# Kernel optimization log

Hardware: AMD Instinct MI355X
Metric: run time of the kernel (lower is better)

The kernel has to match this reference:

```python
import jax, jax.numpy as jnp
import numpy as np

# dims from init_kwargs
B, T = 64, 128
CB, DB = 8, 256
IN_DIM = CB + DB            # 264
H_STATE = 512
NUM_HEADS = 4
NUM_SHIFT = 3
M = 128                     # memory content size (slot width)
A = 2048                    # number of memory addresses
READ_SIZE = NUM_HEADS * M   # 512
PARAMS_PER_HEAD = M + 1 + 1 + NUM_SHIFT + 1 + 2 * M  # key,beta,g,shift,gamma,erase,add = 390
UPDATE_SIZE = NUM_HEADS * PARAMS_PER_HEAD             # 1560
EPS = 1e-8


def setup_inputs() -> dict:
    key = jax.random.key(0)
    ks = jax.random.split(key, 4)
    w = lambda k, sh: jax.random.normal(k, sh, jnp.float32) * 0.02
    return {
        "x": jax.random.normal(ks[0], (B, T, IN_DIM), jnp.float32),
        "W_state": w(ks[1], (IN_DIM + H_STATE + READ_SIZE, H_STATE)),
        "b_state": jnp.zeros((H_STATE,), jnp.float32),
        "W_out": w(ks[2], (H_STATE, DB)),
        "b_out": jnp.zeros((DB,), jnp.float32),
        "W_upd": w(ks[3], (H_STATE, UPDATE_SIZE)),
        "b_upd": jnp.zeros((UPDATE_SIZE,), jnp.float32),
    }


def _ntm_step(params, carry, x_t):
    W_state, b_state, W_out, b_out, W_upd, b_upd = params
    h, wt, mem = carry  # h [B,S], wt [B,H,A], mem [B,M,A]

    # --- read from memory with previous attention ---
    read = jnp.einsum('bma,bha->bhm', mem, wt).reshape(B, READ_SIZE)

    # --- controller ---
    ctrl_in = jnp.concatenate([x_t, h, read], axis=-1)
    h_new = jax.nn.sigmoid(ctrl_in @ W_state + b_state)
    out = jax.nn.sigmoid(h_new @ W_out + b_out)
    upd = (h_new @ W_upd + b_upd).reshape(B, NUM_HEADS, PARAMS_PER_HEAD)

    # --- split interface parameters per head ---
    k_vec = upd[..., :M]                                              # key [B,H,M]
    beta = jax.nn.softplus(upd[..., M:M + 1])                         # key strength
    g = jax.nn.sigmoid(upd[..., M + 1:M + 2])                         # interpolation gate
    shift = jax.nn.softmax(upd[..., M + 2:M + 2 + NUM_SHIFT], axis=-1)
    gamma = 1.0 + jax.nn.softplus(upd[..., M + 2 + NUM_SHIFT:M + 3 + NUM_SHIFT])
    erase = jax.nn.sigmoid(upd[..., M + 3 + NUM_SHIFT:2 * M + 3 + NUM_SHIFT])
    add = jnp.tanh(upd[..., 2 * M + 3 + NUM_SHIFT:])

    # --- content addressing: cosine similarity + sharpened softmax ---
    dots = jnp.einsum('bhm,bma->bha', k_vec, mem)
    k_norm = jnp.linalg.norm(k_vec, axis=-1, keepdims=True)           # [B,H,1]
    m_norm = jnp.linalg.norm(mem, axis=1)[:, None, :]                 # [B,1,A]
    sim = dots / (k_norm * m_norm + EPS)
    wc = jax.nn.softmax(beta * sim, axis=-1)

    # --- gate with previous attention ---
    wg = g * wc + (1.0 - g) * wt

    # --- circular convolutional shift (small fixed loop over NUM_SHIFT) ---
    center = NUM_SHIFT // 2
    shifted = jnp.stack([jnp.roll(wg, s - center, axis=-1) for s in range(NUM_SHIFT)], axis=2)  # [B,H,S,A]
    ws = jnp.einsum('bhs,bhsa->bha', shift, shifted)

    # --- sharpening ---
    wp = jnp.power(ws + EPS, gamma)
    wt_new = wp / jnp.sum(wp, axis=-1, keepdims=True)

    # --- memory erase / add ---
    erase_term = jnp.prod(1.0 - jnp.einsum('bhm,bha->bhma', erase, wt_new), axis=1)  # [B,M,A]
    add_term = jnp.einsum('bhm,bha->bma', add, wt_new)
    mem_new = mem * erase_term + add_term

    return (h_new, wt_new, mem_new), out


def reference(x, W_state, b_state, W_out, b_out, W_upd, b_upd):
    # init_state (matches torch module): h=ones, wt one-hot at address 0, mem=0.01
    h0 = jnp.ones((B, H_STATE), jnp.float32)
    wt0 = jnp.zeros((B, NUM_HEADS, A), jnp.float32).at[:, :, 0].set(1.0)
    mem0 = jnp.full((B, M, A), 0.01, jnp.float32)
    params = (W_state, b_state, W_out, b_out, W_upd, b_upd)

    def step(carry, x_t):
        return _ntm_step(params, carry, x_t)

    _, outs = jax.lax.scan(step, (h0, wt0, mem0), jnp.swapaxes(x, 0, 1))
    return jnp.swapaxes(outs, 0, 1)  # [B, T, DB]
```

## Files before the change

### kernel.cpp

```cpp
#include <hip/hip_runtime.h>
#include <math.h>

#define BB 64
#define TT 128
#define DBX 256
#define IND 264
#define HS 512
#define NH 4
#define MMM 128
#define AAA 2048
#define PPH 390
#define NCOLS (DBX + NH*PPH)
#define KTOT (IND + HS + HS)
#define KSPL 8
#define KCH  161
#define EPSF 1e-8f

__device__ __forceinline__ float sigmf(float x){ return 1.0f/(1.0f+expf(-x)); }
__device__ __forceinline__ float softplusf(float x){ return (x > 20.0f) ? x : log1pf(expf(x)); }

__global__ void k_init(float* __restrict__ hT, float* __restrict__ readT,
                       float* __restrict__ wt, float* __restrict__ mem){
  int i = blockIdx.x*blockDim.x + threadIdx.x;
  int stride = gridDim.x*blockDim.x;
  for (int idx=i; idx<BB*MMM*AAA; idx+=stride) mem[idx]=0.01f;
  for (int idx=i; idx<HS*BB; idx+=stride){ hT[idx]=1.0f; readT[idx]=0.01f; }
  for (int idx=i; idx<BB*NH*AAA; idx+=stride) wt[idx] = ((idx & (AAA-1))==0)?1.0f:0.0f;
}

__global__ __launch_bounds__(256) void k_tx(const float* __restrict__ x, float* __restrict__ xT){
  int b = blockIdx.x;
  for (int f = threadIdx.x; f < TT*IND; f += 256)
    xT[(size_t)f*BB + b] = x[(size_t)b*TT*IND + f];
}

__global__ __launch_bounds__(256) void k1_state(
    const float* __restrict__ xT, const float* __restrict__ Wst,
    const float* __restrict__ hTp, const float* __restrict__ readTp,
    float* __restrict__ hpart, float* __restrict__ wcsum, float* __restrict__ wpsum, int t)
{
  int tid = threadIdx.x, wave = tid>>6, lane = tid&63;
  int ks = blockIdx.y;
  int j0 = blockIdx.x*16 + wave*4;
  if (blockIdx.x==0 && ks==0){
    wcsum[tid] = 0.0f;
    wpsum[tid] = 0.0f;
  }
  float a0=0,a1=0,a2=0,a3=0;
  int k0 = ks*KCH, kend = k0+KCH;

  #define K1STEP(AEXPR) { float aV=(AEXPR); \
      float4 wv = *(const float4*)(Wst + (size_t)k*HS + j0); \
      a0 += aV*wv.x; a1 += aV*wv.y; a2 += aV*wv.z; a3 += aV*wv.w; }

  {int s = k0, e = kend<IND?kend:IND;
   #pragma unroll 4
   for (int k=s;k<e;++k) K1STEP(xT[((size_t)t*IND + k)*BB + lane]); }
  {int s = k0>IND?k0:IND, e = kend<(IND+HS)?kend:(IND+HS);
   #pragma unroll 4
   for (int k=s;k<e;++k) K1STEP(hTp[(k-IND)*BB + lane]); }
  {int s = k0>(IND+HS)?k0:(IND+HS), e = kend;
   #pragma unroll 4
   for (int k=s;k<e;++k) K1STEP(readTp[(k-IND-HS)*BB + lane]); }
  #undef K1STEP

  float* hp = hpart + (size_t)ks*HS*BB + (size_t)j0*BB + lane;
  hp[0]    = a0;
  hp[BB]   = a1;
  hp[2*BB] = a2;
  hp[3*BB] = a3;
}

__global__ __launch_bounds__(512) void k2h(
    const float* __restrict__ hpart, const float* __restrict__ bst, float* __restrict__ hTn)
{
  int idx = blockIdx.x*512 + threadIdx.x;
  float v = 0.0f;
  #pragma unroll
  for (int ks=0; ks<KSPL; ++ks) v += hpart[(size_t)ks*HS*BB + idx];
  hTn[idx] = sigmf(v + bst[idx>>6]);
}

__global__ __launch_bounds__(256) void k2_outupd(
    const float* __restrict__ hTn,
    const float* __restrict__ Wout, const float* __restrict__ bout,
    const float* __restrict__ Wupd, const float* __restrict__ bupd,
    float* __restrict__ out,
    float* __restrict__ kvec_t, float* __restrict__ beta, float* __restrict__ gbuf,
    float* __restrict__ gam, float* __restrict__ shraw,
    float* __restrict__ erase, float* __restrict__ addb, int t)
{
  __shared__ float part[4][8][BB];
  int tid = threadIdx.x, ks = tid>>6, lane = tid&63;
  int c0 = blockIdx.x*8;
  bool isout = (c0 < DBX);
  size_t strd = isout ? (size_t)DBX : (size_t)(NH*PPH);
  const float* wbase = isout ? (Wout + c0) : (Wupd + (c0 - DBX));
  bool valid = (c0 < NCOLS);

  float acc[8] = {0,0,0,0,0,0,0,0};
  if (valid){
    int k0 = ks*128;
    #pragma unroll 4
    for (int k=k0; k<k0+128; ++k){
      float a = hTn[k*BB + lane];
      const float4* w4 = (const float4*)(wbase + (size_t)k*strd);
      float4 wa = w4[0], wb = w4[1];
      acc[0]+=a*wa.x; acc[1]+=a*wa.y; acc[2]+=a*wa.z; acc[3]+=a*wa.w;
      acc[4]+=a*wb.x; acc[5]+=a*wb.y; acc[6]+=a*wb.z; acc[7]+=a*wb.w;
    }
  }
  #pragma unroll
  for (int u=0; u<8; ++u) part[ks][u][lane] = acc[u];
  __syncthreads();
  if (!valid) return;

  for (int idx=tid; idx<8*BB; idx+=256){
    int u = idx>>6, b = idx&63;
    int c = c0+u;
    float v = part[0][u][b] + part[1][u][b] + part[2][u][b] + part[3][u][b];
    if (isout){
      out[((size_t)b*TT + t)*DBX + c] = sigmf(v + bout[c]);
    } else {
      int u2 = c - DBX;
      int hh = u2 / PPH;
      int p  = u2 - hh*PPH;
      v += bupd[u2];
      if (p < MMM)            kvec_t[b*HS + p*NH + hh] = v;
      else if (p == MMM)      beta[b*NH+hh] = softplusf(v);
      else if (p == MMM+1)    gbuf[b*NH+hh] = sigmf(v);
      else if (p <  MMM+5)    shraw[(b*NH+hh)*3 + (p-(MMM+2))] = v;
      else if (p == MMM+5)    gam[b*NH+hh] = 1.0f + softplusf(v);
      else if (p <  2*MMM+6)  erase[b*HS + hh*MMM + (p-(MMM+6))] = sigmf(v);
      else                    addb[b*HS + hh*MMM + (p-(2*MMM+6))] = tanhf(v);
    }
  }
}

__global__ __launch_bounds__(512) void k_dotsP(
    const float* __restrict__ mem, const float* __restrict__ kvec_t,
    float* __restrict__ dpart, float* __restrict__ n2part)
{
  int b = blockIdx.x, s = blockIdx.y, z = blockIdx.z, tid = threadIdx.x;
  __shared__ __align__(16) float klt[128];
  if (tid < 128) klt[tid] = kvec_t[b*HS + z*128 + tid];
  __syncthreads();
  int a = s*512 + tid;
  const float* mp = mem + (size_t)b*MMM*AAA + (size_t)(z*32)*AAA + a;
  const float4* k4 = (const float4*)klt;
  float a0=0,a1=0,a2=0,a3=0,n2=0;
  #pragma unroll 8
  for (int m=0; m<32; ++m){
    float mv = mp[(size_t)m*AAA];
    float4 kv = k4[m];
    a0 += kv.x*mv; a1 += kv.y*mv; a2 += kv.z*mv; a3 += kv.w*mv;
    n2 += mv*mv;
  }
  size_t base = ((size_t)(z*BB+b)*NH)*AAA + a;
  dpart[base]        = a0;
  dpart[base+AAA]    = a1;
  dpart[base+2*AAA]  = a2;
  dpart[base+3*AAA]  = a3;
  n2part[(size_t)(z*BB+b)*AAA + a] = n2;
}

__global__ __launch_bounds__(512) void k_dotsF(
    const float* __restrict__ dpart, const float* __restrict__ n2part,
    const float* __restrict__ kvec_t, const float* __restrict__ beta,
    float* __restrict__ ebuf, float* __restrict__ wcsum)
{
  int b = blockIdx.x, s = blockIdx.y, tid = threadIdx.x;
  __shared__ float red[HS];
  __shared__ float kn[NH];
  __shared__ float rsum[8*NH];
  float kv = kvec_t[b*HS + tid];
  red[tid] = kv*kv;
  __syncthreads();
  #pragma unroll
  for (int off=256; off>=4; off>>=1){
    if (tid < off) red[tid] += red[tid+off];
    __syncthreads();
  }
  if (tid < NH) kn[tid] = sqrtf(red[tid]);
  __syncthreads();

  int a = s*512 + tid;
  float d[NH] = {0,0,0,0};
  float n2 = 0.0f;
  #pragma unroll
  for (int z=0; z<4; ++z){
    size_t base = ((size_t)(z*BB+b)*NH)*AAA + a;
    d[0] += dpart[base];
    d[1] += dpart[base+AAA];
    d[2] += dpart[base+2*AAA];
    d[3] += dpart[base+3*AAA];
    n2   += n2part[(size_t)(z*BB+b)*AAA + a];
  }
  float mn = sqrtf(n2);
  int wid = tid >> 6, lane = tid & 63;
  #pragma unroll
  for (int hh=0; hh<NH; ++hh){
    float sim = d[hh]/(kn[hh]*mn + EPSF);
    float e = expf(beta[b*NH+hh]*sim);
    ebuf[((size_t)(b*NH+hh))*AAA + a] = e;
    float v = e;
    #pragma unroll
    for (int off=32; off>0; off>>=1) v += __shfl_xor(v, off);
    if (lane==0) rsum[wid*NH+hh] = v;
  }
  __syncthreads();
  if (tid < NH){
    float s2 = 0.0f;
    #pragma unroll
    for (int w=0; w<8; ++w) s2 += rsum[w*NH+tid];
    atomicAdd(&wcsum[b*NH+tid], s2);
  }
}

__global__ __launch_bounds__(512) void k_shift(
    const float* __restrict__ ebuf, const float* __restrict__ wcsum,
    const float* __restrict__ gbuf, const float* __restrict__ shraw,
    const float* __restrict__ gam, const float* __restrict__ wt,
    float* __restrict__ wpb, float* __restrict__ wpsum)
{
  int b = blockIdx.x, s = blockIdx.y, tid = threadIdx.x;
  int a = s*512 + tid;
  int am1 = (a + AAA - 1) & (AAA-1);
  int ap1 = (a + 1) & (AAA-1);
  __shared__ float sh[NH*3], gl[NH], gml[NH], winv[NH];
  __shared__ float rsum[8*NH];
  if (tid < NH){
    int hh = tid;
    float s0=shraw[(b*NH+hh)*3], s1=shraw[(b*NH+hh)*3+1], s2=shraw[(b*NH+hh)*3+2];
    float mx = fmaxf(s0, fmaxf(s1, s2));
    float e0=expf(s0-mx), e1=expf(s1-mx), e2=expf(s2-mx);
    float inv = 1.0f/(e0+e1+e2);
    sh[hh*3+0]=e0*inv; sh[hh*3+1]=e1*inv; sh[hh*3+2]=e2*inv;
    gl[hh]  = gbuf[b*NH+hh];
    gml[hh] = gam[b*NH+hh];
    winv[hh]= 1.0f/wcsum[b*NH+hh];
  }
  __syncthreads();
  int wid = tid >> 6, lane = tid & 63;
  #pragma unroll
  for (int hh=0; hh<NH; ++hh){
    const float* eb = ebuf + ((size_t)(b*NH+hh))*AAA;
    const float* wb = wt   + ((size_t)(b*NH+hh))*AAA;
    float inv = winv[hh], g = gl[hh];
    float s0 = sh[hh*3+0], s1 = sh[hh*3+1], s2 = sh[hh*3+2];
    float wgm1 = g*eb[am1]*inv + (1.0f-g)*wb[am1];
    float wg0  = g*eb[a]  *inv + (1.0f-g)*wb[a];
    float wgp1 = g*eb[ap1]*inv + (1.0f-g)*wb[ap1];
    float ws = s0*wgp1 + s1*wg0 + s2*wgm1;
    float wp = powf(ws + EPSF, gml[hh]);
    wpb[((size_t)(b*NH+hh))*AAA + a] = wp;
    float v = wp;
    #pragma unroll
    for (int off=32; off>0; off>>=1) v += __shfl_xor(v, off);
    if (lane==0) rsum[wid*NH+hh] = v;
  }
  __syncthreads();
  if (tid < NH){
    float s3 = 0.0f;
    #pragma unroll
    for (int w=0; w<8; ++w) s3 += rsum[w*NH+tid];
    atomicAdd(&wpsum[b*NH+tid], s3);
  }
}

__global__ __launch_bounds__(512) void k_updAB(
    float* __restrict__ mem, const float* __restrict__ wpb, const float* __restrict__ wpsum,
    const float* __restrict__ erase, const float* __restrict__ addb,
    float* __restrict__ wt, float* __restrict__ readTn)
{
  __shared__ __align__(16) float wl[AAA*4];
  int b = blockIdx.x, my = blockIdx.y, tid = threadIdx.x;
  int wave = tid >> 6, lane = tid & 63;
  float winv[4];
  #pragma unroll
  for (int h=0;h<4;++h) winv[h] = 1.0f/wpsum[b*NH+h];
  #pragma unroll
  for (int c4=0;c4<4;++c4){
    int a = c4*512 + tid;
    float w0 = wpb[((size_t)(b*NH+0))*AAA + a]*winv[0];
    float w1 = wpb[((size_t)(b*NH+1))*AAA + a]*winv[1];
    float w2 = wpb[((size_t)(b*NH+2))*AAA + a]*winv[2];
    float w3 = wpb[((size_t)(b*NH+3))*AAA + a]*winv[3];
    wl[a*4+0]=w0; wl[a*4+1]=w1; wl[a*4+2]=w2; wl[a*4+3]=w3;
    if (my == 0){
      wt[((size_t)(b*NH+0))*AAA + a] = w0;
      wt[((size_t)(b*NH+1))*AAA + a] = w1;
      wt[((size_t)(b*NH+2))*AAA + a] = w2;
      wt[((size_t)(b*NH+3))*AAA + a] = w3;
    }
  }
  __syncthreads();

  int m0 = my*8 + wave, m1 = m0 + 64;
  float er0[4], ad0[4], er1[4], ad1[4];
  #pragma unroll
  for (int h=0;h<4;++h){
    er0[h] = erase[b*HS + h*MMM + m0];
    ad0[h] = addb [b*HS + h*MMM + m0];
    er1[h] = erase[b*HS + h*MMM + m1];
    ad1[h] = addb [b*HS + h*MMM + m1];
  }
  float* row0 = mem + (size_t)b*MMM*AAA + (size_t)m0*AAA;
  float* row1 = mem + (size_t)b*MMM*AAA + (size_t)m1*AAA;
  const float4* wl4 = (const float4*)wl;
  float r00=0,r01=0,r02=0,r03=0, r10=0,r11=0,r12=0,r13=0;
  #pragma unroll 4
  for (int it=0; it<32; ++it){
    int a = it*64 + lane;
    float mv0 = row0[a], mv1 = row1[a];
    float4 w4 = wl4[a];
    float et0 = (1.0f - er0[0]*w4.x)*(1.0f - er0[1]*w4.y)
              * (1.0f - er0[2]*w4.z)*(1.0f - er0[3]*w4.w);
    float at0 = ad0[0]*w4.x + ad0[1]*w4.y + ad0[2]*w4.z + ad0[3]*w4.w;
    float n0 = mv0*et0 + at0;
    row0[a] = n0;
    r00 += n0*w4.x; r01 += n0*w4.y; r02 += n0*w4.z; r03 += n0*w4.w;
    float et1 = (1.0f - er1[0]*w4.x)*(1.0f - er1[1]*w4.y)
              * (1.0f - er1[2]*w4.z)*(1.0f - er1[3]*w4.w);
    float at1 = ad1[0]*w4.x + ad1[1]*w4.y + ad1[2]*w4.z + ad1[3]*w4.w;
    float n1 = mv1*et1 + at1;
    row1[a] = n1;
    r10 += n1*w4.x; r11 += n1*w4.y; r12 += n1*w4.z; r13 += n1*w4.w;
  }
  float rr[2][NH] = {{r00,r01,r02,r03},{r10,r11,r12,r13}};
  #pragma unroll
  for (int q=0; q<2; ++q){
    #pragma unroll
    for (int hh=0; hh<NH; ++hh){
      float v = rr[q][hh];
      #pragma unroll
      for (int off=32; off>0; off>>=1) v += __shfl_xor(v, off);
      rr[q][hh] = v;
    }
  }
  if (lane == 0){
    #pragma unroll
    for (int hh=0; hh<NH; ++hh){
      readTn[(size_t)(hh*MMM+m0)*BB + b] = rr[0][hh];
      readTn[(size_t)(hh*MMM+m1)*BB + b] = rr[1][hh];
    }
  }
}

extern "C" void kernel_launch(void* const* d_in, const int* in_sizes, int n_in,
                              void* d_out, int out_size, void* d_ws, size_t ws_size,
                              hipStream_t stream){
  const float* x    = (const float*)d_in[0];
  const float* Wst  = (const float*)d_in[1];
  const float* bst  = (const float*)d_in[2];
  const float* Wout = (const float*)d_in[3];
  const float* bout = (const float*)d_in[4];
  const float* Wupd = (const float*)d_in[5];
  const float* bupd = (const float*)d_in[6];
  float* out = (float*)d_out;

  float* p = (float*)d_ws;
  float* hT     = p; p += 2*HS*BB;
  float* readT  = p; p += 2*HS*BB;
  float* hpart  = p; p += KSPL*HS*BB;
  float* xT     = p; p += (size_t)TT*IND*BB;
  float* wt     = p; p += BB*NH*AAA;
  float* mem    = p; p += (size_t)BB*MMM*AAA;
  float* kvec_t = p; p += BB*HS;
  float* beta   = p; p += BB*NH;
  float* gbuf   = p; p += BB*NH;
  float* gam    = p; p += BB*NH;
  float* shraw  = p; p += BB*NH*3;
  float* erase  = p; p += BB*HS;
  float* addb   = p; p += BB*HS;
  float* ebuf   = p; p += BB*NH*AAA;
  float* wpb    = p; p += 4*(size_t)BB*NH*AAA;
  float* n2part = p; p += 4*BB*AAA;
  float* wcsum  = p; p += BB*NH;
  float* wpsum  = p; p += BB*NH;
  float* dpart  = wpb;

  k_init<<<2048, 256, 0, stream>>>(hT, readT, wt, mem);
  k_tx<<<BB, 256, 0, stream>>>(x, xT);
  for (int t=0; t<TT; ++t){
    const float* hTp = hT    + (t&1)*HS*BB;
    float* hTn       = hT    + ((t+1)&1)*HS*BB;
    const float* rTp = readT + (t&1)*HS*BB;
    float* rTn       = readT + ((t+1)&1)*HS*BB;
    k1_state<<<dim3(32,KSPL), 256, 0, stream>>>(xT, Wst, hTp, rTp, hpart, wcsum, wpsum, t);
    k2h<<<64, 512, 0, stream>>>(hpart, bst, hTn);
    k2_outupd<<<dim3(259), 256, 0, stream>>>(hTn, Wout, bout, Wupd, bupd, out,
        kvec_t, beta, gbuf, gam, shraw, erase, addb, t);
    k_dotsP<<<dim3(BB,4,4), 512, 0, stream>>>(mem, kvec_t, dpart, n2part);
    k_dotsF<<<dim3(BB,4), 512, 0, stream>>>(dpart, n2part, kvec_t, beta, ebuf, wcsum);
    k_shift<<<dim3(BB,4), 512, 0, stream>>>(ebuf, wcsum, gbuf, shraw, gam, wt, wpb, wpsum);
    k_updAB<<<dim3(BB,8), 512, 0, stream>>>(mem, wpb, wpsum, erase, addb, wt, rTn);
  }
}
```

Baseline: 10.36 ms.

## Fuse dot split-K kernels and move shift/sharpen into memory update kernel

The two-stage content-addressing dots (partial over M chunks, then finalize) become a single kernel that streams all 128 memory rows per address, which removes the dpart/n2part round trip through global memory. The shift, sharpen and normalization steps are folded into the erase/add update kernel, so each of the 8 blocks per batch redundantly recomputes the full attention in shared memory and no longer needs a global wpsum atomic. The wt buffer is double-buffered so the previous attention can be read while the new one is written. This trades two launches and extra global traffic per step for redundant per-block compute and a larger shared-memory footprint (64KB).

```diff
diff --git a/kernel.cpp b/kernel.cpp
--- a/kernel.cpp
+++ b/kernel.cpp
@@ -11,7 +11,6 @@
 #define AAA 2048
 #define PPH 390
 #define NCOLS (DBX + NH*PPH)
-#define KTOT (IND + HS + HS)
 #define KSPL 8
 #define KCH  161
 #define EPSF 1e-8f
@@ -20,12 +19,12 @@
 __device__ __forceinline__ float softplusf(float x){ return (x > 20.0f) ? x : log1pf(expf(x)); }
 
 __global__ void k_init(float* __restrict__ hT, float* __restrict__ readT,
-                       float* __restrict__ wt, float* __restrict__ mem){
+                       float* __restrict__ wt0, float* __restrict__ mem){
   int i = blockIdx.x*blockDim.x + threadIdx.x;
   int stride = gridDim.x*blockDim.x;
   for (int idx=i; idx<BB*MMM*AAA; idx+=stride) mem[idx]=0.01f;
   for (int idx=i; idx<HS*BB; idx+=stride){ hT[idx]=1.0f; readT[idx]=0.01f; }
-  for (int idx=i; idx<BB*NH*AAA; idx+=stride) wt[idx] = ((idx & (AAA-1))==0)?1.0f:0.0f;
+  for (int idx=i; idx<BB*NH*AAA; idx+=stride) wt0[idx] = ((idx & (AAA-1))==0)?1.0f:0.0f;
 }
 
 __global__ __launch_bounds__(256) void k_tx(const float* __restrict__ x, float* __restrict__ xT){
@@ -37,14 +36,13 @@
 __global__ __launch_bounds__(256) void k1_state(
     const float* __restrict__ xT, const float* __restrict__ Wst,
     const float* __restrict__ hTp, const float* __restrict__ readTp,
-    float* __restrict__ hpart, float* __restrict__ wcsum, float* __restrict__ wpsum, int t)
+    float* __restrict__ hpart, float* __restrict__ wcsum, int t)
 {
   int tid = threadIdx.x, wave = tid>>6, lane = tid&63;
   int ks = blockIdx.y;
   int j0 = blockIdx.x*16 + wave*4;
   if (blockIdx.x==0 && ks==0){
     wcsum[tid] = 0.0f;
-    wpsum[tid] = 0.0f;
   }
   float a0=0,a1=0,a2=0,a3=0;
   int k0 = ks*KCH, kend = k0+KCH;
@@ -137,165 +135,155 @@
   }
 }
 
-__global__ __launch_bounds__(512) void k_dotsP(
+__global__ __launch_bounds__(256) void k_dots(
     const float* __restrict__ mem, const float* __restrict__ kvec_t,
-    float* __restrict__ dpart, float* __restrict__ n2part)
-{
-  int b = blockIdx.x, s = blockIdx.y, z = blockIdx.z, tid = threadIdx.x;
-  __shared__ __align__(16) float klt[128];
-  if (tid < 128) klt[tid] = kvec_t[b*HS + z*128 + tid];
-  __syncthreads();
-  int a = s*512 + tid;
-  const float* mp = mem + (size_t)b*MMM*AAA + (size_t)(z*32)*AAA + a;
-  const float4* k4 = (const float4*)klt;
-  float a0=0,a1=0,a2=0,a3=0,n2=0;
-  #pragma unroll 8
-  for (int m=0; m<32; ++m){
-    float mv = mp[(size_t)m*AAA];
-    float4 kv = k4[m];
-    a0 += kv.x*mv; a1 += kv.y*mv; a2 += kv.z*mv; a3 += kv.w*mv;
-    n2 += mv*mv;
-  }
-  size_t base = ((size_t)(z*BB+b)*NH)*AAA + a;
-  dpart[base]        = a0;
-  dpart[base+AAA]    = a1;
-  dpart[base+2*AAA]  = a2;
-  dpart[base+3*AAA]  = a3;
-  n2part[(size_t)(z*BB+b)*AAA + a] = n2;
-}
-
-__global__ __launch_bounds__(512) void k_dotsF(
-    const float* __restrict__ dpart, const float* __restrict__ n2part,
-    const float* __restrict__ kvec_t, const float* __restrict__ beta,
+    const float* __restrict__ beta,
     float* __restrict__ ebuf, float* __restrict__ wcsum)
 {
   int b = blockIdx.x, s = blockIdx.y, tid = threadIdx.x;
-  __shared__ float red[HS];
-  __shared__ float kn[NH];
-  __shared__ float rsum[8*NH];
-  float kv = kvec_t[b*HS + tid];
-  red[tid] = kv*kv;
-  __syncthreads();
-  #pragma unroll
-  for (int off=256; off>=4; off>>=1){
+  __shared__ __align__(16) float kl[HS];
+  __shared__ float red[256];
+  __shared__ float kn[NH], pb[NH];
+  __shared__ float rsum[4*NH];
+  kl[tid]     = kvec_t[b*HS + tid];
+  kl[tid+256] = kvec_t[b*HS + 256 + tid];
+  if (tid < NH) pb[tid] = beta[b*NH + tid];
+  __syncthreads();
+  red[tid] = kl[tid]*kl[tid] + kl[tid+256]*kl[tid+256];
+  __syncthreads();
+  #pragma unroll
+  for (int off=128; off>=4; off>>=1){
     if (tid < off) red[tid] += red[tid+off];
     __syncthreads();
   }
   if (tid < NH) kn[tid] = sqrtf(red[tid]);
   __syncthreads();
 
-  int a = s*512 + tid;
-  float d[NH] = {0,0,0,0};
-  float n2 = 0.0f;
-  #pragma unroll
-  for (int z=0; z<4; ++z){
-    size_t base = ((size_t)(z*BB+b)*NH)*AAA + a;
-    d[0] += dpart[base];
-    d[1] += dpart[base+AAA];
-    d[2] += dpart[base+2*AAA];
-    d[3] += dpart[base+3*AAA];
-    n2   += n2part[(size_t)(z*BB+b)*AAA + a];
+  int a = s*256 + tid;
+  const float* mp = mem + (size_t)b*MMM*AAA + a;
+  const float4* k4 = (const float4*)kl;
+  float d0=0,d1=0,d2=0,d3=0,n2=0;
+  for (int mb=0; mb<MMM; mb+=16){
+    float mv[16];
+    #pragma unroll
+    for (int u=0;u<16;++u) mv[u] = mp[(size_t)(mb+u)*AAA];
+    #pragma unroll
+    for (int u=0;u<16;++u){
+      float4 kv = k4[mb+u];
+      d0 += kv.x*mv[u]; d1 += kv.y*mv[u]; d2 += kv.z*mv[u]; d3 += kv.w*mv[u];
+      n2 += mv[u]*mv[u];
+    }
   }
   float mn = sqrtf(n2);
-  int wid = tid >> 6, lane = tid & 63;
+  float dd[NH] = {d0,d1,d2,d3};
+  int wave = tid >> 6, lane = tid & 63;
+  float e_r[NH];
   #pragma unroll
   for (int hh=0; hh<NH; ++hh){
-    float sim = d[hh]/(kn[hh]*mn + EPSF);
-    float e = expf(beta[b*NH+hh]*sim);
+    float sim = dd[hh]/(kn[hh]*mn + EPSF);
+    float e = expf(pb[hh]*sim);
+    e_r[hh] = e;
     ebuf[((size_t)(b*NH+hh))*AAA + a] = e;
-    float v = e;
+  }
+  #pragma unroll
+  for (int hh=0; hh<NH; ++hh){
+    float v = e_r[hh];
     #pragma unroll
     for (int off=32; off>0; off>>=1) v += __shfl_xor(v, off);
-    if (lane==0) rsum[wid*NH+hh] = v;
+    if (lane==0) rsum[wave*NH+hh] = v;
   }
   __syncthreads();
   if (tid < NH){
-    float s2 = 0.0f;
-    #pragma unroll
-    for (int w=0; w<8; ++w) s2 += rsum[w*NH+tid];
+    float s2 = rsum[tid] + rsum[NH+tid] + rsum[2*NH+tid] + rsum[3*NH+tid];
     atomicAdd(&wcsum[b*NH+tid], s2);
   }
 }
 
-__global__ __launch_bounds__(512) void k_shift(
-    const float* __restrict__ ebuf, const float* __restrict__ wcsum,
-    const float* __restrict__ gbuf, const float* __restrict__ shraw,
-    const float* __restrict__ gam, const float* __restrict__ wt,
-    float* __restrict__ wpb, float* __restrict__ wpsum)
-{
-  int b = blockIdx.x, s = blockIdx.y, tid = threadIdx.x;
-  int a = s*512 + tid;
-  int am1 = (a + AAA - 1) & (AAA-1);
-  int ap1 = (a + 1) & (AAA-1);
-  __shared__ float sh[NH*3], gl[NH], gml[NH], winv[NH];
-  __shared__ float rsum[8*NH];
-  if (tid < NH){
-    int hh = tid;
-    float s0=shraw[(b*NH+hh)*3], s1=shraw[(b*NH+hh)*3+1], s2=shraw[(b*NH+hh)*3+2];
-    float mx = fmaxf(s0, fmaxf(s1, s2));
-    float e0=expf(s0-mx), e1=expf(s1-mx), e2=expf(s2-mx);
-    float inv = 1.0f/(e0+e1+e2);
-    sh[hh*3+0]=e0*inv; sh[hh*3+1]=e1*inv; sh[hh*3+2]=e2*inv;
-    gl[hh]  = gbuf[b*NH+hh];
-    gml[hh] = gam[b*NH+hh];
-    winv[hh]= 1.0f/wcsum[b*NH+hh];
-  }
-  __syncthreads();
-  int wid = tid >> 6, lane = tid & 63;
-  #pragma unroll
-  for (int hh=0; hh<NH; ++hh){
-    const float* eb = ebuf + ((size_t)(b*NH+hh))*AAA;
-    const float* wb = wt   + ((size_t)(b*NH+hh))*AAA;
-    float inv = winv[hh], g = gl[hh];
-    float s0 = sh[hh*3+0], s1 = sh[hh*3+1], s2 = sh[hh*3+2];
-    float wgm1 = g*eb[am1]*inv + (1.0f-g)*wb[am1];
-    float wg0  = g*eb[a]  *inv + (1.0f-g)*wb[a];
-    float wgp1 = g*eb[ap1]*inv + (1.0f-g)*wb[ap1];
-    float ws = s0*wgp1 + s1*wg0 + s2*wgm1;
-    float wp = powf(ws + EPSF, gml[hh]);
-    wpb[((size_t)(b*NH+hh))*AAA + a] = wp;
-    float v = wp;
-    #pragma unroll
-    for (int off=32; off>0; off>>=1) v += __shfl_xor(v, off);
-    if (lane==0) rsum[wid*NH+hh] = v;
-  }
-  __syncthreads();
-  if (tid < NH){
-    float s3 = 0.0f;
-    #pragma unroll
-    for (int w=0; w<8; ++w) s3 += rsum[w*NH+tid];
-    atomicAdd(&wpsum[b*NH+tid], s3);
-  }
-}
-
-__global__ __launch_bounds__(512) void k_updAB(
-    float* __restrict__ mem, const float* __restrict__ wpb, const float* __restrict__ wpsum,
+__global__ __launch_bounds__(512) void k_updfin(
+    float* __restrict__ mem, const float* __restrict__ ebuf,
+    const float* __restrict__ wtp, float* __restrict__ wtn,
+    const float* __restrict__ wcsum, const float* __restrict__ shraw,
+    const float* __restrict__ gbuf, const float* __restrict__ gam,
     const float* __restrict__ erase, const float* __restrict__ addb,
-    float* __restrict__ wt, float* __restrict__ readTn)
-{
-  __shared__ __align__(16) float wl[AAA*4];
+    float* __restrict__ readTn)
+{
+  __shared__ __align__(16) float wgl[AAA*4];
+  __shared__ __align__(16) float wpl[AAA*4];
+  __shared__ float sh[12], gg[4], gmm[4], wci[4], psr[8*4], wpsl[4];
   int b = blockIdx.x, my = blockIdx.y, tid = threadIdx.x;
   int wave = tid >> 6, lane = tid & 63;
-  float winv[4];
-  #pragma unroll
-  for (int h=0;h<4;++h) winv[h] = 1.0f/wpsum[b*NH+h];
-  #pragma unroll
-  for (int c4=0;c4<4;++c4){
+  if (tid < 4){
+    gg[tid]  = gbuf[b*NH+tid];
+    gmm[tid] = gam[b*NH+tid];
+    wci[tid] = 1.0f/wcsum[b*NH+tid];
+    float s0 = shraw[(b*NH+tid)*3], s1 = shraw[(b*NH+tid)*3+1], s2 = shraw[(b*NH+tid)*3+2];
+    float mx = fmaxf(s0, fmaxf(s1, s2));
+    float e0 = expf(s0-mx), e1 = expf(s1-mx), e2 = expf(s2-mx);
+    float inv = 1.0f/(e0+e1+e2);
+    sh[tid*3] = e0*inv; sh[tid*3+1] = e1*inv; sh[tid*3+2] = e2*inv;
+  }
+  __syncthreads();
+  #pragma unroll
+  for (int c4=0; c4<4; ++c4){
     int a = c4*512 + tid;
-    float w0 = wpb[((size_t)(b*NH+0))*AAA + a]*winv[0];
-    float w1 = wpb[((size_t)(b*NH+1))*AAA + a]*winv[1];
-    float w2 = wpb[((size_t)(b*NH+2))*AAA + a]*winv[2];
-    float w3 = wpb[((size_t)(b*NH+3))*AAA + a]*winv[3];
-    wl[a*4+0]=w0; wl[a*4+1]=w1; wl[a*4+2]=w2; wl[a*4+3]=w3;
-    if (my == 0){
-      wt[((size_t)(b*NH+0))*AAA + a] = w0;
-      wt[((size_t)(b*NH+1))*AAA + a] = w1;
-      wt[((size_t)(b*NH+2))*AAA + a] = w2;
-      wt[((size_t)(b*NH+3))*AAA + a] = w3;
-    }
-  }
-  __syncthreads();
-
+    float4 wg;
+    wg.x = gg[0]*ebuf[((size_t)(b*NH+0))*AAA+a]*wci[0] + (1.0f-gg[0])*wtp[((size_t)(b*NH+0))*AAA+a];
+    wg.y = gg[1]*ebuf[((size_t)(b*NH+1))*AAA+a]*wci[1] + (1.0f-gg[1])*wtp[((size_t)(b*NH+1))*AAA+a];
+    wg.z = gg[2]*ebuf[((size_t)(b*NH+2))*AAA+a]*wci[2] + (1.0f-gg[2])*wtp[((size_t)(b*NH+2))*AAA+a];
+    wg.w = gg[3]*ebuf[((size_t)(b*NH+3))*AAA+a]*wci[3] + (1.0f-gg[3])*wtp[((size_t)(b*NH+3))*AAA+a];
+    ((float4*)wgl)[a] = wg;
+  }
+  __syncthreads();
+  float ps0=0,ps1=0,ps2=0,ps3=0;
+  const float4* wg4 = (const float4*)wgl;
+  #pragma unroll
+  for (int c4=0; c4<4; ++c4){
+    int a = c4*512 + tid;
+    int am1 = (a + AAA - 1) & (AAA-1);
+    int ap1 = (a + 1) & (AAA-1);
+    float4 w0 = wg4[a], wm = wg4[am1], wp_ = wg4[ap1];
+    float p0 = powf(sh[0]*wp_.x + sh[1]*w0.x + sh[2]*wm.x + EPSF, gmm[0]);
+    float p1 = powf(sh[3]*wp_.y + sh[4]*w0.y + sh[5]*wm.y + EPSF, gmm[1]);
+    float p2 = powf(sh[6]*wp_.z + sh[7]*w0.z + sh[8]*wm.z + EPSF, gmm[2]);
+    float p3 = powf(sh[9]*wp_.w + sh[10]*w0.w + sh[11]*wm.w + EPSF, gmm[3]);
+    ((float4*)wpl)[a] = make_float4(p0,p1,p2,p3);
+    ps0 += p0; ps1 += p1; ps2 += p2; ps3 += p3;
+  }
+  {
+    float ps[4] = {ps0,ps1,ps2,ps3};
+    #pragma unroll
+    for (int h=0; h<4; ++h){
+      float v = ps[h];
+      #pragma unroll
+      for (int off=32; off>0; off>>=1) v += __shfl_xor(v, off);
+      if (lane==0) psr[wave*4+h] = v;
+    }
+    __syncthreads();
+    if (tid < 4){
+      float s = 0.0f;
+      #pragma unroll
+      for (int w=0; w<8; ++w) s += psr[w*4+tid];
+      wpsl[tid] = 1.0f/s;
+    }
+    __syncthreads();
+  }
+  {
+    float wi0=wpsl[0], wi1=wpsl[1], wi2=wpsl[2], wi3=wpsl[3];
+    #pragma unroll
+    for (int c4=0; c4<4; ++c4){
+      int a = c4*512 + tid;
+      float4 wv = ((const float4*)wpl)[a];
+      wv.x *= wi0; wv.y *= wi1; wv.z *= wi2; wv.w *= wi3;
+      ((float4*)wpl)[a] = wv;
+      if (my == 0){
+        wtn[((size_t)(b*NH+0))*AAA + a] = wv.x;
+        wtn[((size_t)(b*NH+1))*AAA + a] = wv.y;
+        wtn[((size_t)(b*NH+2))*AAA + a] = wv.z;
+        wtn[((size_t)(b*NH+3))*AAA + a] = wv.w;
+      }
+    }
+  }
+  __syncthreads();
   int m0 = my*8 + wave, m1 = m0 + 64;
   float er0[4], ad0[4], er1[4], ad1[4];
   #pragma unroll
@@ -307,7 +295,7 @@
   }
   float* row0 = mem + (size_t)b*MMM*AAA + (size_t)m0*AAA;
   float* row1 = mem + (size_t)b*MMM*AAA + (size_t)m1*AAA;
-  const float4* wl4 = (const float4*)wl;
+  const float4* wl4 = (const float4*)wpl;
   float r00=0,r01=0,r02=0,r03=0, r10=0,r11=0,r12=0,r13=0;
   #pragma unroll 4
   for (int it=0; it<32; ++it){
@@ -364,7 +352,7 @@
   float* readT  = p; p += 2*HS*BB;
   float* hpart  = p; p += KSPL*HS*BB;
   float* xT     = p; p += (size_t)TT*IND*BB;
-  float* wt     = p; p += BB*NH*AAA;
+  float* wtb    = p; p += 2*BB*NH*AAA;
   float* mem    = p; p += (size_t)BB*MMM*AAA;
   float* kvec_t = p; p += BB*HS;
   float* beta   = p; p += BB*NH;
@@ -374,26 +362,23 @@
   float* erase  = p; p += BB*HS;
   float* addb   = p; p += BB*HS;
   float* ebuf   = p; p += BB*NH*AAA;
-  float* wpb    = p; p += 4*(size_t)BB*NH*AAA;
-  float* n2part = p; p += 4*BB*AAA;
   float* wcsum  = p; p += BB*NH;
-  float* wpsum  = p; p += BB*NH;
-  float* dpart  = wpb;
-
-  k_init<<<2048, 256, 0, stream>>>(hT, readT, wt, mem);
+
+  k_init<<<2048, 256, 0, stream>>>(hT, readT, wtb, mem);
   k_tx<<<BB, 256, 0, stream>>>(x, xT);
   for (int t=0; t<TT; ++t){
     const float* hTp = hT    + (t&1)*HS*BB;
     float* hTn       = hT    + ((t+1)&1)*HS*BB;
     const float* rTp = readT + (t&1)*HS*BB;
     float* rTn       = readT + ((t+1)&1)*HS*BB;
-    k1_state<<<dim3(32,KSPL), 256, 0, stream>>>(xT, Wst, hTp, rTp, hpart, wcsum, wpsum, t);
+    const float* wtp = wtb   + (t&1)*BB*NH*AAA;
+    float* wtn       = wtb   + ((t+1)&1)*BB*NH*AAA;
+    k1_state<<<dim3(32,KSPL), 256, 0, stream>>>(xT, Wst, hTp, rTp, hpart, wcsum, t);
     k2h<<<64, 512, 0, stream>>>(hpart, bst, hTn);
     k2_outupd<<<dim3(259), 256, 0, stream>>>(hTn, Wout, bout, Wupd, bupd, out,
         kvec_t, beta, gbuf, gam, shraw, erase, addb, t);
-    k_dotsP<<<dim3(BB,4,4), 512, 0, stream>>>(mem, kvec_t, dpart, n2part);
-    k_dotsF<<<dim3(BB,4), 512, 0, stream>>>(dpart, n2part, kvec_t, beta, ebuf, wcsum);
-    k_shift<<<dim3(BB,4), 512, 0, stream>>>(ebuf, wcsum, gbuf, shraw, gam, wt, wpb, wpsum);
-    k_updAB<<<dim3(BB,8), 512, 0, stream>>>(mem, wpb, wpsum, erase, addb, wt, rTn);
-  }
-}
+    k_dots<<<dim3(BB,8), 256, 0, stream>>>(mem, kvec_t, beta, ebuf, wcsum);
+    k_updfin<<<dim3(BB,8), 512, 0, stream>>>(mem, ebuf, wtp, wtn, wcsum, shraw,
+        gbuf, gam, erase, addb, rTn);
+  }
+}
```

After: 11.39 ms. +10.0%, slower.
